# Kernel optimization log

Measured on AMD Instinct MI355X. Metric: run time of the kernel, lower is better.

Reference implementation:

```python
import jax, jax.numpy as jnp
import numpy as np
import math

B, C, H, W = 8, 128, 64, 64
R = 16  # reduced channels = C // reduction


def setup_inputs() -> dict:
    key = jax.random.key(0)
    ks = jax.random.split(key, 10)
    s = 0.05
    return {
        "x": jax.random.normal(ks[0], (B, C, H, W), dtype=jnp.float32),
        "Wq": jax.random.normal(ks[1], (R, C), dtype=jnp.float32) * s,
        "bq": jax.random.normal(ks[2], (R,), dtype=jnp.float32) * s,
        "Wk": jax.random.normal(ks[3], (R, C), dtype=jnp.float32) * s,
        "bk": jax.random.normal(ks[4], (R,), dtype=jnp.float32) * s,
        "Wv": jax.random.normal(ks[5], (C, C), dtype=jnp.float32) * s,
        "bv": jax.random.normal(ks[6], (C,), dtype=jnp.float32) * s,
        "Wo": jax.random.normal(ks[7], (C, C), dtype=jnp.float32) * s,
        "bo": jax.random.normal(ks[8], (C,), dtype=jnp.float32) * s,
        "gamma": jax.random.normal(ks[9], (1,), dtype=jnp.float32),
    }


def reference(x, Wq, bq, Wk, bk, Wv, bv, Wo, bo, gamma):
    b, c, h, w = x.shape
    n = h * w
    xf = x.reshape(b, c, n)  # [B, C, N]
    # 1x1 convs are channel-mixing matmuls
    q = jnp.einsum('rc,bcn->bnr', Wq, xf) + bq            # [B, N, R]
    k = jnp.einsum('rc,bcn->brn', Wk, xf) + bk[:, None]    # [B, R, N]
    v = jnp.einsum('oc,bcn->bon', Wv, xf) + bv[:, None]    # [B, C, N]
    scale = 1.0 / math.sqrt(R)
    attn = jax.nn.softmax(jnp.einsum('bnr,brm->bnm', q, k) * scale, axis=-1)  # [B, N, N]
    out = jnp.einsum('bcm,bnm->bcn', v, attn)              # value @ attn^T
    out = jnp.einsum('oc,bcn->bon', Wo, out) + bo[:, None]
    out = gamma[0] * out + xf
    return out.reshape(b, c, h, w)
```

## Files before the change

kernel.cpp:

```cpp
#include <hip/hip_runtime.h>

typedef __bf16 bf16_t;
typedef __attribute__((ext_vector_type(8))) __bf16 bf16x8;
typedef __attribute__((ext_vector_type(16))) float f32x16;
typedef __attribute__((ext_vector_type(2))) unsigned u32x2;
typedef long long i64;
typedef __attribute__((ext_vector_type(2))) long long i64x2;
typedef unsigned long long u64;

#define MFMA32(A, B, C) __builtin_amdgcn_mfma_f32_32x32x16_bf16((A), (B), (C), 0, 0, 0)


__device__ __forceinline__ float fexp2(float x) { return __builtin_amdgcn_exp2f(x); }

__device__ __forceinline__ f32x16 mfma_fp8(i64 a, i64 b, f32x16 c) {
  return __builtin_amdgcn_mfma_f32_32x32x16_fp8_fp8(a, b, c, 0, 0, 0);
}
__device__ __forceinline__ unsigned pk4(float a, float b, float c, float d) {
  unsigned u = __builtin_amdgcn_cvt_pk_fp8_f32(a, b, 0u, false);
  return __builtin_amdgcn_cvt_pk_fp8_f32(c, d, u, true);
}
__device__ __forceinline__ void swap32(unsigned &a, unsigned &b) {
  asm volatile("v_permlane32_swap_b32 %0, %1" : "+v"(a), "+v"(b));
}
__device__ __forceinline__ float xhalf(float x, int hi) {
  unsigned a = __builtin_bit_cast(unsigned, x), b = a;
  asm volatile("v_permlane32_swap_b32 %0, %1" : "+v"(a), "+v"(b));
  return __builtin_bit_cast(float, hi ? a : b);
}
__device__ __forceinline__ unsigned pkbf2(float a, float b) {
  union { bf16_t h[2]; unsigned u; } r;
  r.h[0] = (bf16_t)a; r.h[1] = (bf16_t)b;
  return r.u;
}

__global__ __launch_bounds__(256) void k_qkv(
    const float* __restrict__ x,
    const float* __restrict__ Wq, const float* __restrict__ bq,
    const float* __restrict__ Wk, const float* __restrict__ bk,
    const float* __restrict__ Wv, const float* __restrict__ bv,
    const float* __restrict__ Wo,
    bf16_t* __restrict__ q, bf16_t* __restrict__ kT, char* __restrict__ vfout,
    bf16_t* __restrict__ Wob) {
  __shared__ __align__(16) bf16_t xt[64 * 136];
  __shared__ __align__(16) bf16_t Wqk_s[32 * 136];
  __shared__ __align__(16) bf16_t Wv_s[128 * 152];
  __shared__ __align__(8)  char   vst[128 * 72];
  const float QS = 0.25f * 1.44269504f;
  const int b = blockIdx.y;
  const int nb = blockIdx.x;
  const int n0 = nb * 64;
  const int t = threadIdx.x;
  if (b == 0) {
    int i = nb * 256 + t;
    Wob[i] = (bf16_t)Wo[i];
  }
  for (int i = t; i < 32 * 128; i += 256) {
    int row = i >> 7, col = i & 127;
    float val = (row < 16) ? QS * Wq[row * 128 + col] : Wk[(row - 16) * 128 + col];
    Wqk_s[row * 136 + col] = (bf16_t)val;
  }
  for (int i = t; i < 128 * 128; i += 256)
    Wv_s[(i >> 7) * 152 + (i & 127)] = (bf16_t)Wv[i];

  const int nl = t & 63, cg = t >> 6;
  const float* xb = x + (size_t)b * 524288 + n0 + nl;
  float xv[32];
#pragma unroll
  for (int i = 0; i < 32; ++i) xv[i] = xb[(size_t)(cg * 32 + i) * 4096];
  char* xrow = (char*)xt + nl * 272 + cg * 64;
#pragma unroll
  for (int i = 0; i < 16; ++i)
    *(unsigned*)(xrow + 4 * i) = pkbf2(xv[2 * i], xv[2 * i + 1]);
  __syncthreads();

  const int w = t >> 6, l = t & 63, l31 = l & 31, hi = l >> 5;
  const int nc = w & 1, role = w >> 1;
  const int nloc = nc * 32 + l31;

  f32x16 aqk;
  f32x16 av[2];
#pragma unroll
  for (int i = 0; i < 16; ++i) { aqk[i] = 0.f; av[0][i] = 0.f; av[1][i] = 0.f; }
#pragma unroll
  for (int kk = 0; kk < 8; ++kk) {
    bf16x8 xf = *(const bf16x8*)((char*)xt + nloc * 272 + kk * 32 + hi * 16);
    if (role == 0) {
      bf16x8 wqk = *(const bf16x8*)(&Wqk_s[l31 * 136 + kk * 16 + 8 * hi]);
      aqk = MFMA32(xf, wqk, aqk);
    }
#pragma unroll
    for (int j = 0; j < 2; ++j) {
      int ct = role * 2 + j;
      bf16x8 wvv = *(const bf16x8*)(&Wv_s[(ct * 32 + l31) * 152 + kk * 16 + 8 * hi]);
      av[j] = MFMA32(wvv, xf, av[j]);
    }
  }
  if (role == 0) {
    const float bias_qk = (l31 < 16) ? QS * bq[l31] : bk[l31 - 16];
#pragma unroll
    for (int r = 0; r < 16; ++r) {
      int n = n0 + nc * 32 + (r & 3) + 8 * (r >> 2) + 4 * hi;
      bf16_t vb16 = (bf16_t)(aqk[r] + bias_qk);
      if (l31 < 16) q[((size_t)(b * 4096 + n)) * 16 + l31] = vb16;
      else          kT[((size_t)(b * 4096 + n)) * 16 + (l31 - 16)] = vb16;
    }
  }

  const int mloc = nc * 32 + l31;
#pragma unroll
  for (int j = 0; j < 2; ++j) {
    int ct = role * 2 + j;
#pragma unroll
    for (int r = 0; r < 16; r += 2) {
      int c = ct * 32 + (r & 3) + 8 * (r >> 2) + 4 * hi;
      unsigned pw = pk4(av[j][r] + bv[c], av[j][r + 1] + bv[c + 1], 0.f, 0.f);
      vst[c * 72 + mloc] = (char)(pw & 0xff);
      vst[(c + 1) * 72 + mloc] = (char)((pw >> 8) & 0xff);
    }
  }
  __syncthreads();
  char* vfb = vfout + (size_t)b * 524288 + (size_t)nb * 8192;
#pragma unroll
  for (int it = 0; it < 4; ++it) {
    int id = t + 256 * it;
    int jj = id & 7, ln = (id >> 3) & 63, sl = id >> 9;
    int half = jj >> 2, ct = jj & 3;
    int c = ct * 32 + (ln & 31);
    int m0 = sl * 32 + half * 16 + (ln >> 5) * 8;
    u64 v8 = *(const u64*)(vst + c * 72 + m0);
    *(u64*)(vfb + (size_t)sl * 4096 + (size_t)(jj >> 1) * 1024 + (size_t)ln * 16 + (jj & 1) * 8) = v8;
  }
}

__global__ __launch_bounds__(512, 4) void k_attn(
    const bf16_t* __restrict__ q, const bf16_t* __restrict__ kT,
    const char* __restrict__ vf, const bf16_t* __restrict__ Wob,
    const float* __restrict__ bo, const float* __restrict__ gammap,
    const float* __restrict__ x, float* __restrict__ out) {
  __shared__ __align__(16) bf16_t accb[8][32][136];
  __shared__ float lsum[8][32];
  __shared__ float linv[64];
  const int bid = blockIdx.x;
  const int b = bid & 7, qb = bid >> 3;
  const int t = threadIdx.x, w = t >> 6, l = t & 63, l31 = l & 31, hi = l >> 5;
  const int qg = w & 1, mq = w >> 1;
  const int n0 = qb * 64 + qg * 32;

  const bf16_t* kw = kT + (size_t)b * 65536 + (size_t)mq * 16384;
  const char* vw = vf + (size_t)b * 524288 + (size_t)mq * 131072 + (size_t)l * 16;

  bf16x8 qf = *(const bf16x8*)(q + ((size_t)(b * 4096) + n0 + l31) * 16 + 8 * hi);
  bf16x8 kf = *(const bf16x8*)(kw + (size_t)l31 * 16 + 8 * hi);

  f32x16 z;
#pragma unroll
  for (int i = 0; i < 16; ++i) z[i] = 0.f;
  f32x16 acc[4];
#pragma unroll
  for (int ct = 0; ct < 4; ++ct) acc[ct] = z;
  float lac = 0.f;

#pragma unroll 2
  for (int s = 0; s < 32; ++s) {
    const char* vt = vw + (size_t)s * 4096;
    i64x2 va2[4];
#pragma unroll
    for (int p = 0; p < 4; ++p) va2[p] = *(const i64x2*)(vt + p * 1024);

    f32x16 st = MFMA32(kf, qf, z);
    kf = *(const bf16x8*)(kw + ((size_t)((s + 1) * 32 + l31)) * 16 + 8 * hi);

    float p[16];
#pragma unroll
    for (int i = 0; i < 16; ++i) p[i] = fexp2(st[i]);
    float s0 = (p[0] + p[1]) + (p[2] + p[3]), s1 = (p[4] + p[5]) + (p[6] + p[7]);
    float s2 = (p[8] + p[9]) + (p[10] + p[11]), s3 = (p[12] + p[13]) + (p[14] + p[15]);
    lac += (s0 + s1) + (s2 + s3);

    unsigned w0 = pk4(p[0], p[1], p[2], p[3]);
    unsigned w1 = pk4(p[4], p[5], p[6], p[7]);
    unsigned w2 = pk4(p[8], p[9], p[10], p[11]);
    unsigned w3 = pk4(p[12], p[13], p[14], p[15]);
    swap32(w0, w1);
    swap32(w2, w3);
    u32x2 A, Bv;
    A[0] = w0; A[1] = w1;
    Bv[0] = w2; Bv[1] = w3;
    i64 pA = __builtin_bit_cast(i64, A);
    i64 pB = __builtin_bit_cast(i64, Bv);

#pragma unroll
    for (int ct = 0; ct < 4; ++ct) acc[ct] = mfma_fp8(va2[ct >> 1][ct & 1], pA, acc[ct]);
#pragma unroll
    for (int ct = 0; ct < 4; ++ct) acc[ct] = mfma_fp8(va2[2 + (ct >> 1)][ct & 1], pB, acc[ct]);
  }

  float lT = lac + xhalf(lac, hi);
  if (hi == 0) lsum[w][l31] = lT;
#pragma unroll
  for (int ct = 0; ct < 4; ++ct) {
#pragma unroll
    for (int g = 0; g < 4; ++g) {
      union { unsigned short h[4]; u64 u; } pw;
#pragma unroll
      for (int j = 0; j < 4; ++j) {
        bf16_t bb = (bf16_t)acc[ct][g * 4 + j];
        pw.h[j] = __builtin_bit_cast(unsigned short, bb);
      }
      *(u64*)&accb[w][l31][ct * 32 + 8 * g + 4 * hi] = pw.u;
    }
  }
  __syncthreads();

  {
    const int rn64 = t >> 3;
    const int qg2 = rn64 >> 5, rn = rn64 & 31;
    const int c0 = (t & 7) * 16;
    float L = (lsum[qg2][rn] + lsum[qg2 + 2][rn]) + (lsum[qg2 + 4][rn] + lsum[qg2 + 6][rn]);
    if ((t & 7) == 0) linv[rn64] = 1.0f / L;
    float o[16];
#pragma unroll
    for (int i = 0; i < 16; ++i) o[i] = 0.f;
#pragma unroll
    for (int m2 = 0; m2 < 4; ++m2) {
#pragma unroll
      for (int h2 = 0; h2 < 2; ++h2) {
        bf16x8 ch = *(const bf16x8*)&accb[qg2 + 2 * m2][rn][c0 + h2 * 8];
#pragma unroll
        for (int e = 0; e < 8; ++e) o[h2 * 8 + e] += (float)ch[e];
      }
    }
#pragma unroll
    for (int h2 = 0; h2 < 2; ++h2) {
      bf16x8 sv;
#pragma unroll
      for (int e = 0; e < 8; ++e) sv[e] = (bf16_t)o[h2 * 8 + e];
      *(bf16x8*)&accb[qg2][rn][c0 + h2 * 8] = sv;
    }
  }
  __syncthreads();

  {
    const int obk = w >> 1, nh = w & 1;
    const int o0 = obk * 32;
    f32x16 oc;
#pragma unroll
    for (int i = 0; i < 16; ++i) oc[i] = 0.f;
#pragma unroll
    for (int kk = 0; kk < 8; ++kk) {
      bf16x8 wof = *(const bf16x8*)(Wob + (size_t)(o0 + l31) * 128 + kk * 16 + 8 * hi);
      bf16x8 cf = *(const bf16x8*)&accb[nh][l31][kk * 16 + 8 * hi];
      oc = MFMA32(wof, cf, oc);
    }
    const float g = gammap[0];
    const float iv = linv[nh * 32 + l31];
    const int ng = qb * 64 + nh * 32 + l31;
#pragma unroll
    for (int r = 0; r < 16; ++r) {
      int o_ = o0 + (r & 3) + 8 * (r >> 2) + 4 * hi;
      size_t off = ((size_t)(b * 128 + o_)) * 4096 + ng;
      __builtin_nontemporal_store(g * (oc[r] * iv + bo[o_]) + x[off], &out[off]);
    }
  }
}

extern "C" void kernel_launch(void* const* d_in, const int* in_sizes, int n_in,
                              void* d_out, int out_size, void* d_ws, size_t ws_size,
                              hipStream_t stream) {
  const float* x  = (const float*)d_in[0];
  const float* Wq = (const float*)d_in[1];
  const float* bq = (const float*)d_in[2];
  const float* Wk = (const float*)d_in[3];
  const float* bk = (const float*)d_in[4];
  const float* Wv = (const float*)d_in[5];
  const float* bv = (const float*)d_in[6];
  const float* Wo = (const float*)d_in[7];
  const float* bo = (const float*)d_in[8];
  const float* gm = (const float*)d_in[9];
  float* out = (float*)d_out;

  char* ws = (char*)d_ws;
  bf16_t* q   = (bf16_t*)(ws);
  bf16_t* kT  = (bf16_t*)(ws + (size_t)(1 << 20));
  char*   vf  = (char*)  (ws + (size_t)(2 << 20));
  bf16_t* Wob = (bf16_t*)(ws + (size_t)(6 << 20));

  k_qkv<<<dim3(64, 8), 256, 0, stream>>>(x, Wq, bq, Wk, bk, Wv, bv, Wo, q, kT, vf, Wob);
  k_attn<<<512, 512, 0, stream>>>(q, kT, vf, Wob, bo, gm, x, out);
}
```

Measured before the change: 60.07 us.

## Stage V tiles into LDS with async triple-buffered global_load_lds

Each wave used to load its FP8 V fragments straight from global memory into registers, so the two query-group waves sharing a value slice fetched the same data twice. Now the whole block cooperatively streams V tiles into a triple-buffered LDS ring using global_load_lds, prefetching two steps ahead, and every wave reads its fragments from LDS. The ring reuses the accb buffer that the epilogue needs later. This halves redundant global traffic and overlaps V fetches with compute, but it adds a block-wide barrier every iteration and relies on the async LDS writes completing before that barrier.

```diff
diff --git a/kernel.cpp b/kernel.cpp
--- a/kernel.cpp
+++ b/kernel.cpp
@@ -32,6 +32,11 @@
   union { bf16_t h[2]; unsigned u; } r;
   r.h[0] = (bf16_t)a; r.h[1] = (bf16_t)b;
   return r.u;
+}
+__device__ __forceinline__ void gl_lds16(const void* g, void* l) {
+  __builtin_amdgcn_global_load_lds(
+      (const __attribute__((address_space(1))) void*)g,
+      (__attribute__((address_space(3))) void*)l, 16, 0, 0);
 }
 
 __global__ __launch_bounds__(256) void k_qkv(
@@ -148,11 +153,25 @@
   const int n0 = qb * 64 + qg * 32;
 
   const bf16_t* kw = kT + (size_t)b * 65536 + (size_t)mq * 16384;
-  const char* vw = vf + (size_t)b * 524288 + (size_t)mq * 131072 + (size_t)l * 16;
 
   bf16x8 qf = *(const bf16x8*)(q + ((size_t)(b * 4096) + n0 + l31) * 16 + 8 * hi);
   bf16x8 kf = *(const bf16x8*)(kw + (size_t)l31 * 16 + 8 * hi);
 
+  char* const vls = (char*)&accb[0][0][0];
+  char* r0 = vls;
+  char* r1 = vls + 16384;
+  char* r2 = vls + 32768;
+  const char* vsrc = vf + (size_t)b * 524288;
+  const int ch0 = w * 2, ch1 = w * 2 + 1;
+  const size_t go0 = (size_t)(ch0 >> 2) * 131072 + (size_t)(ch0 & 3) * 1024 + (size_t)l * 16;
+  const size_t go1 = (size_t)(ch1 >> 2) * 131072 + (size_t)(ch1 & 3) * 1024 + (size_t)l * 16;
+  const int lo0 = (ch0 >> 2) * 4096 + (ch0 & 3) * 1024;
+  const int lo1 = (ch1 >> 2) * 4096 + (ch1 & 3) * 1024;
+  gl_lds16(vsrc + go0, r0 + lo0);
+  gl_lds16(vsrc + go1, r0 + lo1);
+  gl_lds16(vsrc + go0 + 4096, r1 + lo0);
+  gl_lds16(vsrc + go1 + 4096, r1 + lo1);
+
   f32x16 z;
 #pragma unroll
   for (int i = 0; i < 16; ++i) z[i] = 0.f;
@@ -163,10 +182,17 @@
 
 #pragma unroll 2
   for (int s = 0; s < 32; ++s) {
-    const char* vt = vw + (size_t)s * 4096;
+    __syncthreads();
+    const char* vt = r0 + mq * 4096 + (size_t)l * 16;
     i64x2 va2[4];
 #pragma unroll
-    for (int p = 0; p < 4; ++p) va2[p] = *(const i64x2*)(vt + p * 1024);
+    for (int pp = 0; pp < 4; ++pp) va2[pp] = *(const i64x2*)(vt + pp * 1024);
+
+    if (s < 30) {
+      size_t go = (size_t)(s + 2) * 4096;
+      gl_lds16(vsrc + go0 + go, r2 + lo0);
+      gl_lds16(vsrc + go1 + go, r2 + lo1);
+    }
 
     f32x16 st = MFMA32(kf, qf, z);
     kf = *(const bf16x8*)(kw + ((size_t)((s + 1) * 32 + l31)) * 16 + 8 * hi);
@@ -194,7 +220,10 @@
     for (int ct = 0; ct < 4; ++ct) acc[ct] = mfma_fp8(va2[ct >> 1][ct & 1], pA, acc[ct]);
 #pragma unroll
     for (int ct = 0; ct < 4; ++ct) acc[ct] = mfma_fp8(va2[2 + (ct >> 1)][ct & 1], pB, acc[ct]);
-  }
+
+    char* tmp = r0; r0 = r1; r1 = r2; r2 = tmp;
+  }
+  __syncthreads();
 
   float lT = lac + xhalf(lac, hi);
   if (hi == 0) lsum[w][l31] = lT;
```

Result: no change. 59.09 us (-1.6%).
